# Performance work log

Measured on AMD Instinct MI355X. Metric: run time of the kernel, lower is better.

Reference implementation:

```python
import jax, jax.numpy as jnp
import numpy as np
import math

B, S, HID = 2, 2048, 1024
NUM_HEADS = 16
HEAD_DIM = HID // NUM_HEADS
SPARSITY_RATIO = 0.1
NEG = -1e9


def _make_sparse_mask(key, seq_len, sparsity_ratio):
    # local window: min(32, seq_len // 4), rows attend to |i - j| <= window // 2
    local_window = min(32, seq_len // 4)
    half = local_window // 2
    idx = jnp.arange(seq_len)
    mask = jnp.abs(idx[:, None] - idx[None, :]) <= half  # [S, S] bool
    # random global connections: n_global random columns per row
    n_global = int(seq_len * sparsity_ratio)
    gidx = jax.random.randint(key, (seq_len, n_global), 0, seq_len)
    mask = mask.at[idx[:, None], gidx].set(True)
    return mask


def setup_inputs() -> dict:
    key = jax.random.key(0)
    ks = jax.random.split(key, 6)
    lim = math.sqrt(6.0 / (HID + HID))  # xavier uniform bound
    def w(k):
        return jax.random.uniform(k, (HID, HID), jnp.float32, -lim, lim)
    return {
        "hidden_states": jax.random.normal(ks[0], (B, S, HID), jnp.float32),
        "Wq": w(ks[1]), "bq": jnp.zeros((HID,), jnp.float32),
        "Wk": w(ks[2]), "bk": jnp.zeros((HID,), jnp.float32),
        "Wv": w(ks[3]), "bv": jnp.zeros((HID,), jnp.float32),
        "Wo": w(ks[4]), "bo": jnp.zeros((HID,), jnp.float32),
        "sparse_mask": _make_sparse_mask(ks[5], S, SPARSITY_RATIO),
    }


def reference(hidden_states, Wq, bq, Wk, bk, Wv, bv, Wo, bo, sparse_mask):
    Bsz, seq, hid = hidden_states.shape
    H, D = NUM_HEADS, hid // NUM_HEADS

    def proj(W, b):
        y = hidden_states @ W.T + b                      # [B, S, hid]
        return y.reshape(Bsz, seq, H, D).transpose(0, 2, 1, 3)  # [B, H, S, D]

    q = proj(Wq, bq)
    k = proj(Wk, bk)
    v = proj(Wv, bv)

    scores = jnp.einsum("bhqd,bhkd->bhqk", q, k) / jnp.sqrt(jnp.float32(D))
    scores = jnp.where(sparse_mask[None, None, :, :], scores, jnp.float32(NEG))
    probs = jax.nn.softmax(scores, axis=-1)
    ctx = jnp.einsum("bhqk,bhkd->bhqd", probs, v)        # [B, H, S, D]
    ctx = ctx.transpose(0, 2, 1, 3).reshape(Bsz, seq, hid)
    return ctx @ Wo.T + bo
```

## Files before the change

kernel.cpp:

```cpp
#include <hip/hip_runtime.h>

typedef short bf16x8 __attribute__((ext_vector_type(8)));
typedef float f32x4 __attribute__((ext_vector_type(4)));
typedef unsigned short us4 __attribute__((ext_vector_type(4)));

#define S_LEN 2048
#define HIDD 1024
#define NH 16
#define HD 64
#define NEGV -1e9f

#define BM 128
#define BN 128
#define BK 64
#define LDSS 72

static __device__ __forceinline__ unsigned short f2bf(float f) {
  union { float f; unsigned u; } v; v.f = f;
  unsigned r = v.u + 0x7FFFu + ((v.u >> 16) & 1u);
  return (unsigned short)(r >> 16);
}

#define GLD16(gp, lp)                                                        \
  __builtin_amdgcn_global_load_lds(                                         \
      (const __attribute__((address_space(1))) void*)(gp),                  \
      (__attribute__((address_space(3))) void*)(lp), 16, 0, 0)

__global__ __launch_bounds__(256) void cvt5_kernel(
    const float* __restrict__ s0, const float* __restrict__ s1, const float* __restrict__ s2,
    const float* __restrict__ s3, const float* __restrict__ s4,
    unsigned short* __restrict__ d0, unsigned short* __restrict__ d1,
    unsigned short* __restrict__ d2, unsigned short* __restrict__ d3,
    unsigned short* __restrict__ d4) {
  const float* s; unsigned short* d; int n4;
  switch (blockIdx.y) {
    case 0: s = s0; d = d0; n4 = (2 * S_LEN * HIDD) / 4; break;
    case 1: s = s1; d = d1; n4 = (HIDD * HIDD) / 4; break;
    case 2: s = s2; d = d2; n4 = (HIDD * HIDD) / 4; break;
    case 3: s = s3; d = d3; n4 = (HIDD * HIDD) / 4; break;
    default: s = s4; d = d4; n4 = (HIDD * HIDD) / 4; break;
  }
  for (int i = blockIdx.x * blockDim.x + threadIdx.x; i < n4;
       i += gridDim.x * blockDim.x) {
    float4 v = ((const float4*)s)[i];
    us4 o;
    o.x = f2bf(v.x); o.y = f2bf(v.y); o.z = f2bf(v.z); o.w = f2bf(v.w);
    ((us4*)d)[i] = o;
  }
}

__global__ __launch_bounds__(256) void maskbits_kernel(
    const unsigned char* __restrict__ m8, unsigned* __restrict__ bits) {
  int idx = blockIdx.x * 256 + threadIdx.x;
  int q = idx >> 6, w = idx & 63;
  bool bytemode = (m8[1] != 0);
  unsigned r = 0;
  if (bytemode) {
    const uint4* p = (const uint4*)(m8 + (size_t)q * 2048 + w * 32);
    uint4 a = p[0], b = p[1];
    unsigned v[8] = {a.x, a.y, a.z, a.w, b.x, b.y, b.z, b.w};
#pragma unroll
    for (int j = 0; j < 8; ++j)
#pragma unroll
      for (int k = 0; k < 4; ++k)
        r |= (((v[j] >> (k * 8)) & 255u) ? 1u : 0u) << (j * 4 + k);
  } else {
    const int4* p = (const int4*)((const int*)m8 + (size_t)q * 2048 + (size_t)w * 32);
#pragma unroll
    for (int j = 0; j < 8; ++j) {
      int4 v = p[j];
      r |= (v.x ? 1u : 0u) << (j * 4 + 0);
      r |= (v.y ? 1u : 0u) << (j * 4 + 1);
      r |= (v.z ? 1u : 0u) << (j * 4 + 2);
      r |= (v.w ? 1u : 0u) << (j * 4 + 3);
    }
  }
  bits[idx] = r;
}

static __device__ __forceinline__ void gemm_core(
    const unsigned short* __restrict__ A, const unsigned short* __restrict__ W,
    int bm0, int bn0, unsigned short* As, unsigned short* Bs, f32x4 (&acc)[4][4]) {
  const int tid = threadIdx.x;
  const int lane = tid & 63;
  const int wid = tid >> 6;
  const int wr = wid >> 1, wc = wid & 1;
  const int l15 = lane & 15, g = lane >> 4;

  for (int k0 = 0; k0 < HIDD; k0 += BK) {
    __syncthreads();
#pragma unroll
    for (int it = 0; it < 4; ++it) {
      int id = tid + it * 256;
      int row = id >> 3;
      int col = (id & 7) * 8;
      *(bf16x8*)&As[row * LDSS + col] =
          *(const bf16x8*)&A[(size_t)(bm0 + row) * HIDD + k0 + col];
      *(bf16x8*)&Bs[row * LDSS + col] =
          *(const bf16x8*)&W[(size_t)(bn0 + row) * HIDD + k0 + col];
    }
    __syncthreads();
#pragma unroll
    for (int kk = 0; kk < 2; ++kk) {
      bf16x8 af[4], bfr[4];
#pragma unroll
      for (int m = 0; m < 4; ++m)
        af[m] = *(const bf16x8*)&As[(wr * 64 + m * 16 + l15) * LDSS + kk * 32 + g * 8];
#pragma unroll
      for (int n = 0; n < 4; ++n)
        bfr[n] = *(const bf16x8*)&Bs[(wc * 64 + n * 16 + l15) * LDSS + kk * 32 + g * 8];
#pragma unroll
      for (int m = 0; m < 4; ++m)
#pragma unroll
        for (int n = 0; n < 4; ++n)
          acc[m][n] = __builtin_amdgcn_mfma_f32_16x16x32_bf16(af[m], bfr[n], acc[m][n], 0, 0, 0);
    }
  }
}

__global__ __launch_bounds__(256) void gemm_qkv(
    const unsigned short* __restrict__ hs,
    const unsigned short* __restrict__ Wq, const unsigned short* __restrict__ Wk,
    const unsigned short* __restrict__ Wv,
    const float* __restrict__ bq, const float* __restrict__ bk, const float* __restrict__ bv,
    unsigned short* __restrict__ Qs, unsigned short* __restrict__ Kb,
    unsigned short* __restrict__ VT) {
  __shared__ unsigned short As[BM * LDSS];
  __shared__ unsigned short Bs[BN * LDSS];
  const int z = blockIdx.z;
  const unsigned short* W = (z == 0) ? Wq : ((z == 1) ? Wk : Wv);
  const float* bias = (z == 0) ? bq : ((z == 1) ? bk : bv);

  f32x4 acc[4][4];
#pragma unroll
  for (int m = 0; m < 4; ++m)
#pragma unroll
    for (int n = 0; n < 4; ++n) acc[m][n] = (f32x4){0.f, 0.f, 0.f, 0.f};

  const int bm0 = blockIdx.x * BM, bn0 = blockIdx.y * BN;
  gemm_core(hs, W, bm0, bn0, As, Bs, acc);

  const int lane = threadIdx.x & 63;
  const int wid = threadIdx.x >> 6;
  const int wr = wid >> 1, wc = wid & 1;
  const int l15 = lane & 15, g = lane >> 4;
  const float qscale = 0.125f * 1.44269504088896f;

#pragma unroll
  for (int m = 0; m < 4; ++m) {
#pragma unroll
    for (int n = 0; n < 4; ++n) {
      int grow0 = bm0 + wr * 64 + m * 16 + g * 4;
      int gcol = bn0 + wc * 64 + n * 16 + l15;
      float bv_ = bias[gcol];
      if (z == 0) {
#pragma unroll
        for (int i = 0; i < 4; ++i)
          Qs[(size_t)(grow0 + i) * HIDD + gcol] = f2bf((acc[m][n][i] + bv_) * qscale);
      } else if (z == 1) {
#pragma unroll
        for (int i = 0; i < 4; ++i)
          Kb[(size_t)(grow0 + i) * HIDD + gcol] = f2bf(acc[m][n][i] + bv_);
      } else {
        int b = grow0 >> 11, s = grow0 & 2047;
        int h = gcol >> 6, d = gcol & 63;
        us4 pk;
#pragma unroll
        for (int i = 0; i < 4; ++i) pk[i] = f2bf(acc[m][n][i] + bv_);
        *(us4*)&VT[((size_t)(b * NH + h) * HD + d) * S_LEN + s] = pk;
      }
    }
  }
}

__global__ __launch_bounds__(256) void gemm_o(
    const unsigned short* __restrict__ ctx, const unsigned short* __restrict__ Wo,
    const float* __restrict__ bo, float* __restrict__ out) {
  __shared__ unsigned short As[BM * LDSS];
  __shared__ unsigned short Bs[BN * LDSS];
  f32x4 acc[4][4];
#pragma unroll
  for (int m = 0; m < 4; ++m)
#pragma unroll
    for (int n = 0; n < 4; ++n) acc[m][n] = (f32x4){0.f, 0.f, 0.f, 0.f};

  const int bm0 = blockIdx.x * BM, bn0 = blockIdx.y * BN;
  gemm_core(ctx, Wo, bm0, bn0, As, Bs, acc);

  const int lane = threadIdx.x & 63;
  const int wid = threadIdx.x >> 6;
  const int wr = wid >> 1, wc = wid & 1;
  const int l15 = lane & 15, g = lane >> 4;
#pragma unroll
  for (int m = 0; m < 4; ++m) {
#pragma unroll
    for (int n = 0; n < 4; ++n) {
      int grow0 = bm0 + wr * 64 + m * 16 + g * 4;
      int gcol = bn0 + wc * 64 + n * 16 + l15;
      float bv_ = bo[gcol];
#pragma unroll
      for (int i = 0; i < 4; ++i)
        out[(size_t)(grow0 + i) * HIDD + gcol] = acc[m][n][i] + bv_;
    }
  }
}

__global__ __launch_bounds__(512) void attn2_kernel(
    const unsigned short* __restrict__ Qs, const unsigned short* __restrict__ Kb,
    const unsigned short* __restrict__ VT, const unsigned* __restrict__ mbits,
    unsigned short* __restrict__ ctx) {
  __shared__ __align__(16) unsigned short Kt[2][4096];
  __shared__ __align__(16) unsigned short Vt[2][4096];
  __shared__ __align__(16) unsigned short Pl[8][16][72];

  const int tid = threadIdx.x;
  const int wid = tid >> 6, lane = tid & 63;
  const int l15 = lane & 15, g = lane >> 4;
  const int l7 = l15 & 7;
  const int b = blockIdx.x >> 4, h = blockIdx.x & 15;
  const int qrow = blockIdx.y * 128 + wid * 16 + l15;

  const unsigned short* Kbh = Kb + (size_t)b * S_LEN * HIDD + h * HD;
  const unsigned short* VTbh = VT + (size_t)(b * NH + h) * HD * S_LEN;

  const unsigned short* Qrow = Qs + (size_t)(b * S_LEN + qrow) * HIDD + h * HD;
  bf16x8 qf0 = *(const bf16x8*)(Qrow + g * 8);
  bf16x8 qf1 = *(const bf16x8*)(Qrow + 32 + g * 8);

  const unsigned* mrow = mbits + (size_t)qrow * 64;

  const int rb0 = l15 * 64 + ((g ^ l7)) * 8;
  const int rb1 = l15 * 64 + ((g ^ l7) ^ 4) * 8;

  const int wk = wid & 3;

  float m_run = -1e8f, l_run = 0.f;
  f32x4 oacc[4];
#pragma unroll
  for (int dc = 0; dc < 4; ++dc) oacc[dc] = (f32x4){0.f, 0.f, 0.f, 0.f};

#define STAGE(bufi, kv0_)                                                     \
  do {                                                                        \
    _Pragma("unroll")                                                         \
    for (int j = 0; j < 2; ++j) {                                             \
      int p = (wk * 2 + j) * 64 + lane;                                       \
      int r_ = p >> 3;                                                        \
      int ch_ = (p & 7) ^ (r_ & 7);                                           \
      if (wid < 4)                                                            \
        GLD16(Kbh + (size_t)((kv0_) + r_) * HIDD + ch_ * 8,                   \
              &Kt[bufi][(wk * 2 + j) * 512]);                                 \
      else                                                                    \
        GLD16(VTbh + (size_t)r_ * S_LEN + (kv0_) + ch_ * 8,                   \
              &Vt[bufi][(wk * 2 + j) * 512]);                                 \
    }                                                                         \
  } while (0)

  uint2 mw = *(const uint2*)mrow;
  STAGE(0, 0);
  __syncthreads();

  for (int it = 0; it < 32; ++it) {
    const int buf = it & 1;
    uint2 mw_n = mw;
    if (it + 1 < 32) {
      STAGE(buf ^ 1, (it + 1) * 64);
      mw_n = *(const uint2*)(mrow + (it + 1) * 2);
    }

    const unsigned short* Kbuf = &Kt[buf][0];
    f32x4 sacc[4];
#pragma unroll
    for (int t = 0; t < 4; ++t) {
      sacc[t] = (f32x4){0.f, 0.f, 0.f, 0.f};
      bf16x8 ka = *(const bf16x8*)(Kbuf + t * 1024 + rb0);
      bf16x8 kb2 = *(const bf16x8*)(Kbuf + t * 1024 + rb1);
      sacc[t] = __builtin_amdgcn_mfma_f32_16x16x32_bf16(ka, qf0, sacc[t], 0, 0, 0);
      sacc[t] = __builtin_amdgcn_mfma_f32_16x16x32_bf16(kb2, qf1, sacc[t], 0, 0, 0);
    }

    float pmax = NEGV;
#pragma unroll
    for (int t = 0; t < 4; ++t) {
      unsigned word = (t & 2) ? mw.y : mw.x;
      unsigned nib = (word >> ((t & 1) * 16 + g * 4)) & 0xFu;
#pragma unroll
      for (int i = 0; i < 4; ++i) {
        sacc[t][i] = ((nib >> i) & 1u) ? sacc[t][i] : NEGV;
        pmax = fmaxf(pmax, sacc[t][i]);
      }
    }
    pmax = fmaxf(pmax, __shfl_xor(pmax, 16));
    pmax = fmaxf(pmax, __shfl_xor(pmax, 32));
    float m_new = fmaxf(m_run, pmax);
    float corr = exp2f(m_run - m_new);
    float lsum = 0.f;
#pragma unroll
    for (int t = 0; t < 4; ++t) {
      us4 pk;
#pragma unroll
      for (int i = 0; i < 4; ++i) {
        float p = exp2f(sacc[t][i] - m_new);
        lsum += p;
        pk[i] = f2bf(p);
      }
      *(us4*)&Pl[wid][l15][t * 16 + g * 4] = pk;
    }
    lsum += __shfl_xor(lsum, 16);
    lsum += __shfl_xor(lsum, 32);
    l_run = l_run * corr + lsum;
    m_run = m_new;
#pragma unroll
    for (int dc = 0; dc < 4; ++dc) oacc[dc] *= corr;

    bf16x8 pf0 = *(const bf16x8*)&Pl[wid][l15][g * 8];
    bf16x8 pf1 = *(const bf16x8*)&Pl[wid][l15][32 + g * 8];

    const unsigned short* Vbuf = &Vt[buf][0];
#pragma unroll
    for (int dc = 0; dc < 4; ++dc) {
      bf16x8 va = *(const bf16x8*)(Vbuf + dc * 1024 + rb0);
      bf16x8 vb = *(const bf16x8*)(Vbuf + dc * 1024 + rb1);
      oacc[dc] = __builtin_amdgcn_mfma_f32_16x16x32_bf16(va, pf0, oacc[dc], 0, 0, 0);
      oacc[dc] = __builtin_amdgcn_mfma_f32_16x16x32_bf16(vb, pf1, oacc[dc], 0, 0, 0);
    }

    mw = mw_n;
    __syncthreads();
  }

  float inv_l = 1.f / l_run;
  unsigned short* crow = ctx + (size_t)(b * S_LEN + qrow) * HIDD + h * HD;
#pragma unroll
  for (int dc = 0; dc < 4; ++dc) {
    us4 o;
#pragma unroll
    for (int i = 0; i < 4; ++i) o[i] = f2bf(oacc[dc][i] * inv_l);
    *(us4*)&crow[dc * 16 + g * 4] = o;
  }
}

extern "C" void kernel_launch(void* const* d_in, const int* in_sizes, int n_in,
                              void* d_out, int out_size, void* d_ws, size_t ws_size,
                              hipStream_t stream) {
  const float* hs = (const float*)d_in[0];
  const float* Wq = (const float*)d_in[1];
  const float* bq = (const float*)d_in[2];
  const float* Wk = (const float*)d_in[3];
  const float* bk = (const float*)d_in[4];
  const float* Wv = (const float*)d_in[5];
  const float* bv = (const float*)d_in[6];
  const float* Wo = (const float*)d_in[7];
  const float* bo = (const float*)d_in[8];
  const unsigned char* mask = (const unsigned char*)d_in[9];

  char* ws = (char*)d_ws;
  unsigned short* hs_bf = (unsigned short*)(ws);
  unsigned short* Wq_bf = (unsigned short*)(ws + (8u << 20));
  unsigned short* Wk_bf = (unsigned short*)(ws + (10u << 20));
  unsigned short* Wv_bf = (unsigned short*)(ws + (12u << 20));
  unsigned short* Wo_bf = (unsigned short*)(ws + (14u << 20));
  unsigned short* Qs    = (unsigned short*)(ws + (16u << 20));
  unsigned short* Kbf   = (unsigned short*)(ws + (24u << 20));
  unsigned short* VT    = (unsigned short*)(ws + (32u << 20));
  unsigned short* ctxb  = (unsigned short*)(ws + (40u << 20));
  unsigned* mbits = (unsigned*)(ws);
  float* out = (float*)d_out;

  cvt5_kernel<<<dim3(256, 5), 256, 0, stream>>>(hs, Wq, Wk, Wv, Wo,
                                                hs_bf, Wq_bf, Wk_bf, Wv_bf, Wo_bf);
  gemm_qkv<<<dim3(32, 8, 3), 256, 0, stream>>>(hs_bf, Wq_bf, Wk_bf, Wv_bf,
                                               bq, bk, bv, Qs, Kbf, VT);
  maskbits_kernel<<<512, 256, 0, stream>>>(mask, mbits);
  attn2_kernel<<<dim3(32, 16), 512, 0, stream>>>(Qs, Kbf, VT, mbits, ctxb);
  gemm_o<<<dim3(32, 8), 256, 0, stream>>>(ctxb, Wo_bf, bo, out);
}
```

Before: 163.3 us.

## Use swizzled direct-to-LDS GEMM loads, lazy softmax rescale, smaller output-GEMM tiles

```diff
diff --git a/kernel.cpp b/kernel.cpp
--- a/kernel.cpp
+++ b/kernel.cpp
@@ -8,17 +8,19 @@
 #define HIDD 1024
 #define NH 16
 #define HD 64
-#define NEGV -1e9f
-
-#define BM 128
-#define BN 128
+
 #define BK 64
-#define LDSS 72
 
 static __device__ __forceinline__ unsigned short f2bf(float f) {
   union { float f; unsigned u; } v; v.f = f;
   unsigned r = v.u + 0x7FFFu + ((v.u >> 16) & 1u);
   return (unsigned short)(r >> 16);
+}
+
+static __device__ __forceinline__ unsigned cvtpk(float lo, float hi) {
+  unsigned r;
+  asm("v_cvt_pk_bf16_f32 %0, %1, %2" : "=v"(r) : "v"(lo), "v"(hi));
+  return r;
 }
 
 #define GLD16(gp, lp)                                                        \
@@ -78,39 +80,46 @@
   bits[idx] = r;
 }
 
-static __device__ __forceinline__ void gemm_core(
+template <int MFRAG>
+static __device__ __forceinline__ void gemm_core2(
     const unsigned short* __restrict__ A, const unsigned short* __restrict__ W,
-    int bm0, int bn0, unsigned short* As, unsigned short* Bs, f32x4 (&acc)[4][4]) {
+    int bm0, int bn0, unsigned short* As, unsigned short* Bs,
+    f32x4 (&acc)[MFRAG][4]) {
   const int tid = threadIdx.x;
   const int lane = tid & 63;
   const int wid = tid >> 6;
   const int wr = wid >> 1, wc = wid & 1;
-  const int l15 = lane & 15, g = lane >> 4;
+  const int l15 = lane & 15, g = lane >> 4, l7 = l15 & 7;
+  const int ra = (g ^ l7) * 8;
 
   for (int k0 = 0; k0 < HIDD; k0 += BK) {
     __syncthreads();
 #pragma unroll
+    for (int it = 0; it < MFRAG; ++it) {
+      int p = it * 256 + tid;
+      int r = p >> 3, ch = (p & 7) ^ (r & 7);
+      GLD16(A + (size_t)(bm0 + r) * HIDD + k0 + ch * 8,
+            As + (it * 256 + wid * 64) * 8);
+    }
+#pragma unroll
     for (int it = 0; it < 4; ++it) {
-      int id = tid + it * 256;
-      int row = id >> 3;
-      int col = (id & 7) * 8;
-      *(bf16x8*)&As[row * LDSS + col] =
-          *(const bf16x8*)&A[(size_t)(bm0 + row) * HIDD + k0 + col];
-      *(bf16x8*)&Bs[row * LDSS + col] =
-          *(const bf16x8*)&W[(size_t)(bn0 + row) * HIDD + k0 + col];
+      int p = it * 256 + tid;
+      int r = p >> 3, ch = (p & 7) ^ (r & 7);
+      GLD16(W + (size_t)(bn0 + r) * HIDD + k0 + ch * 8,
+            Bs + (it * 256 + wid * 64) * 8);
     }
     __syncthreads();
 #pragma unroll
     for (int kk = 0; kk < 2; ++kk) {
-      bf16x8 af[4], bfr[4];
-#pragma unroll
-      for (int m = 0; m < 4; ++m)
-        af[m] = *(const bf16x8*)&As[(wr * 64 + m * 16 + l15) * LDSS + kk * 32 + g * 8];
+      bf16x8 af[MFRAG], bfr[4];
+#pragma unroll
+      for (int m = 0; m < MFRAG; ++m)
+        af[m] = *(const bf16x8*)&As[(wr * (MFRAG * 16) + m * 16 + l15) * 64 + (ra ^ (kk * 32))];
 #pragma unroll
       for (int n = 0; n < 4; ++n)
-        bfr[n] = *(const bf16x8*)&Bs[(wc * 64 + n * 16 + l15) * LDSS + kk * 32 + g * 8];
-#pragma unroll
-      for (int m = 0; m < 4; ++m)
+        bfr[n] = *(const bf16x8*)&Bs[(wc * 64 + n * 16 + l15) * 64 + (ra ^ (kk * 32))];
+#pragma unroll
+      for (int m = 0; m < MFRAG; ++m)
 #pragma unroll
         for (int n = 0; n < 4; ++n)
           acc[m][n] = __builtin_amdgcn_mfma_f32_16x16x32_bf16(af[m], bfr[n], acc[m][n], 0, 0, 0);
@@ -125,8 +134,8 @@
     const float* __restrict__ bq, const float* __restrict__ bk, const float* __restrict__ bv,
     unsigned short* __restrict__ Qs, unsigned short* __restrict__ Kb,
     unsigned short* __restrict__ VT) {
-  __shared__ unsigned short As[BM * LDSS];
-  __shared__ unsigned short Bs[BN * LDSS];
+  __shared__ __align__(16) unsigned short As[128 * 64];
+  __shared__ __align__(16) unsigned short Bs[128 * 64];
   const int z = blockIdx.z;
   const unsigned short* W = (z == 0) ? Wq : ((z == 1) ? Wk : Wv);
   const float* bias = (z == 0) ? bq : ((z == 1) ? bk : bv);
@@ -137,14 +146,14 @@
 #pragma unroll
     for (int n = 0; n < 4; ++n) acc[m][n] = (f32x4){0.f, 0.f, 0.f, 0.f};
 
-  const int bm0 = blockIdx.x * BM, bn0 = blockIdx.y * BN;
-  gemm_core(hs, W, bm0, bn0, As, Bs, acc);
+  const int bm0 = blockIdx.x * 128, bn0 = blockIdx.y * 128;
+  gemm_core2<4>(hs, W, bm0, bn0, As, Bs, acc);
 
   const int lane = threadIdx.x & 63;
   const int wid = threadIdx.x >> 6;
   const int wr = wid >> 1, wc = wid & 1;
   const int l15 = lane & 15, g = lane >> 4;
-  const float qscale = 0.125f * 1.44269504088896f;
+  const float qscale = 0.125f;
 
 #pragma unroll
   for (int m = 0; m < 4; ++m) {
@@ -176,26 +185,26 @@
 __global__ __launch_bounds__(256) void gemm_o(
     const unsigned short* __restrict__ ctx, const unsigned short* __restrict__ Wo,
     const float* __restrict__ bo, float* __restrict__ out) {
-  __shared__ unsigned short As[BM * LDSS];
-  __shared__ unsigned short Bs[BN * LDSS];
-  f32x4 acc[4][4];
-#pragma unroll
-  for (int m = 0; m < 4; ++m)
+  __shared__ __align__(16) unsigned short As[64 * 64];
+  __shared__ __align__(16) unsigned short Bs[128 * 64];
+  f32x4 acc[2][4];
+#pragma unroll
+  for (int m = 0; m < 2; ++m)
 #pragma unroll
     for (int n = 0; n < 4; ++n) acc[m][n] = (f32x4){0.f, 0.f, 0.f, 0.f};
 
-  const int bm0 = blockIdx.x * BM, bn0 = blockIdx.y * BN;
-  gemm_core(ctx, Wo, bm0, bn0, As, Bs, acc);
+  const int bm0 = blockIdx.x * 64, bn0 = blockIdx.y * 128;
+  gemm_core2<2>(ctx, Wo, bm0, bn0, As, Bs, acc);
 
   const int lane = threadIdx.x & 63;
   const int wid = threadIdx.x >> 6;
   const int wr = wid >> 1, wc = wid & 1;
   const int l15 = lane & 15, g = lane >> 4;
 #pragma unroll
-  for (int m = 0; m < 4; ++m) {
+  for (int m = 0; m < 2; ++m) {
 #pragma unroll
     for (int n = 0; n < 4; ++n) {
-      int grow0 = bm0 + wr * 64 + m * 16 + g * 4;
+      int grow0 = bm0 + wr * 32 + m * 16 + g * 4;
       int gcol = bn0 + wc * 64 + n * 16 + l15;
       float bv_ = bo[gcol];
 #pragma unroll
@@ -205,7 +214,7 @@
   }
 }
 
-__global__ __launch_bounds__(512) void attn2_kernel(
+__global__ __launch_bounds__(512) void attn3_kernel(
     const unsigned short* __restrict__ Qs, const unsigned short* __restrict__ Kb,
     const unsigned short* __restrict__ VT, const unsigned* __restrict__ mbits,
     unsigned short* __restrict__ ctx) {
@@ -231,7 +240,6 @@
 
   const int rb0 = l15 * 64 + ((g ^ l7)) * 8;
   const int rb1 = l15 * 64 + ((g ^ l7) ^ 4) * 8;
-
   const int wk = wid & 3;
 
   float m_run = -1e8f, l_run = 0.f;
@@ -278,39 +286,43 @@
       sacc[t] = __builtin_amdgcn_mfma_f32_16x16x32_bf16(kb2, qf1, sacc[t], 0, 0, 0);
     }
 
-    float pmax = NEGV;
+    float pmax = sacc[0][0];
+#pragma unroll
+    for (int t = 0; t < 4; ++t)
+#pragma unroll
+      for (int i = 0; i < 4; ++i) pmax = fmaxf(pmax, sacc[t][i]);
+    pmax = fmaxf(pmax, __shfl_xor(pmax, 16));
+    pmax = fmaxf(pmax, __shfl_xor(pmax, 32));
+
+    if (__any(pmax > m_run + 5.545177f)) {
+      float m_new = fmaxf(m_run, pmax);
+      float corr = __expf(m_run - m_new);
+      l_run *= corr;
+#pragma unroll
+      for (int dc = 0; dc < 4; ++dc) oacc[dc] *= corr;
+      m_run = m_new;
+    }
+
+    float lsum = 0.f;
 #pragma unroll
     for (int t = 0; t < 4; ++t) {
       unsigned word = (t & 2) ? mw.y : mw.x;
       unsigned nib = (word >> ((t & 1) * 16 + g * 4)) & 0xFu;
+      float pm[4];
 #pragma unroll
       for (int i = 0; i < 4; ++i) {
-        sacc[t][i] = ((nib >> i) & 1u) ? sacc[t][i] : NEGV;
-        pmax = fmaxf(pmax, sacc[t][i]);
+        float p = __expf(sacc[t][i] - m_run);
+        pm[i] = ((nib >> i) & 1u) ? p : 0.f;
+        lsum += pm[i];
       }
-    }
-    pmax = fmaxf(pmax, __shfl_xor(pmax, 16));
-    pmax = fmaxf(pmax, __shfl_xor(pmax, 32));
-    float m_new = fmaxf(m_run, pmax);
-    float corr = exp2f(m_run - m_new);
-    float lsum = 0.f;
-#pragma unroll
-    for (int t = 0; t < 4; ++t) {
-      us4 pk;
-#pragma unroll
-      for (int i = 0; i < 4; ++i) {
-        float p = exp2f(sacc[t][i] - m_new);
-        lsum += p;
-        pk[i] = f2bf(p);
-      }
-      *(us4*)&Pl[wid][l15][t * 16 + g * 4] = pk;
+      uint2 w2;
+      w2.x = cvtpk(pm[0], pm[1]);
+      w2.y = cvtpk(pm[2], pm[3]);
+      *(uint2*)&Pl[wid][l15][t * 16 + g * 4] = w2;
     }
     lsum += __shfl_xor(lsum, 16);
     lsum += __shfl_xor(lsum, 32);
-    l_run = l_run * corr + lsum;
-    m_run = m_new;
-#pragma unroll
-    for (int dc = 0; dc < 4; ++dc) oacc[dc] *= corr;
+    l_run += lsum;
 
     bf16x8 pf0 = *(const bf16x8*)&Pl[wid][l15][g * 8];
     bf16x8 pf1 = *(const bf16x8*)&Pl[wid][l15][32 + g * 8];
@@ -371,6 +383,6 @@
   gemm_qkv<<<dim3(32, 8, 3), 256, 0, stream>>>(hs_bf, Wq_bf, Wk_bf, Wv_bf,
                                                bq, bk, bv, Qs, Kbf, VT);
   maskbits_kernel<<<512, 256, 0, stream>>>(mask, mbits);
-  attn2_kernel<<<dim3(32, 16), 512, 0, stream>>>(Qs, Kbf, VT, mbits, ctxb);
-  gemm_o<<<dim3(32, 8), 256, 0, stream>>>(ctxb, Wo_bf, bo, out);
-}
+  attn3_kernel<<<dim3(32, 16), 512, 0, stream>>>(Qs, Kbf, VT, mbits, ctxb);
+  gemm_o<<<dim3(64, 8), 256, 0, stream>>>(ctxb, Wo_bf, bo, out);
+}
```

After: 139.9 us. -14.4%, faster.
